# Kernel tuning notes

Hardware: AMD Instinct MI355X
Metric: run time of the kernel (lower is better)

## Reference

```python
import jax, jax.numpy as jnp
import numpy as np

B, T, NX = 2, 2048, 512
H = 2                    # n_head (structurally forced to 2 by rns() broadcasting)
L = 64                   # num landmarks (cfg.MODEL.LANDMARK)
K = 32                   # rns neighbors per token
HD = NX // H // 2        # differential head dim = 128
EPS = 1e-5


def setup_inputs() -> dict:
    key = jax.random.key(0)
    ks = jax.random.split(key, 16)
    inp = {}
    inp["x"] = jax.random.normal(ks[0], (B, T, NX), jnp.float32)
    # linear weights (torch nn.Linear stores [out,in], applies x @ W.T)
    inp["wq"] = jax.random.normal(ks[1], (NX, NX), jnp.float32) * 0.02
    inp["wk"] = jax.random.normal(ks[2], (NX, NX), jnp.float32) * 0.02
    inp["wv"] = jax.random.normal(ks[3], (NX, NX), jnp.float32) * 0.02
    inp["wo"] = jax.random.normal(ks[4], (NX, NX), jnp.float32) * 0.02
    # landmark modulation params (kaiming-normal-ish init)
    inp["m1"] = jax.random.normal(ks[5], (2 * H, L, 1), jnp.float32)
    inp["m2"] = jax.random.normal(ks[6], (2 * H, 1, L), jnp.float32)
    # differential-attention lambda params
    inp["lq1"] = jax.random.normal(ks[7], (HD,), jnp.float32) * 0.1
    inp["lk1"] = jax.random.normal(ks[8], (HD,), jnp.float32) * 0.1
    inp["lq2"] = jax.random.normal(ks[9], (HD,), jnp.float32) * 0.1
    inp["lk2"] = jax.random.normal(ks[10], (HD,), jnp.float32) * 0.1
    inp["rms_g"] = jnp.ones((2 * HD,), jnp.float32)
    inp["l"] = 3  # layer depth for lambda_init_fn
    inp["num_landmark"] = L
    inp["rns_indices"] = jax.random.randint(ks[11], (B, T, K), 0, T)
    # random.sample(range(t), L) -> distinct indices
    inp["landmark"] = jax.random.permutation(ks[12], T)[:L]
    return inp


def _forward(x, wq, wk, wv, wo, m1, m2, lq1, lk1, lq2, lk2, rms_g,
             l, rns_indices, landmark):
    b, t, nx = x.shape
    hd = nx // H // 2
    q = x @ wq.T
    k = x @ wk.T
    v = x @ wv.T
    qh = q.reshape(b, t, 2 * H, hd).transpose(0, 2, 1, 3)   # [b,2H,t,hd]
    kh = k.reshape(b, t, 2 * H, hd).transpose(0, 2, 3, 1)   # [b,2H,hd,t]
    vh = v.reshape(b, t, H, 2 * hd).transpose(0, 2, 1, 3)   # [b,H,t,2hd]

    # landmark (Nystrom) low-rank factors, L2-normalized over head dim
    sq = qh[:, :, landmark, :]                               # [b,2H,L,hd]
    sk = kh[:, :, :, landmark]                               # [b,2H,hd,L]
    sq = sq / jnp.linalg.norm(sq, axis=3, keepdims=True)
    sk = sk / jnp.linalg.norm(sk, axis=2, keepdims=True)
    sq = m1[None] * sq
    sk = m2[None] * sk

    w1 = jnp.matmul(qh, sk)                                  # [b,2H,t,L]
    w2 = jnp.matmul(sq, kh)                                  # [b,2H,L,t]
    w = jnp.matmul(w1, w2)                                   # [b,2H,t,t]

    lam_init = 0.8 - 0.6 * np.exp(-0.3 * l)
    lam = jnp.exp(jnp.sum(lq1 * lk1)) - jnp.exp(jnp.sum(lq2 * lk2)) + lam_init

    # rns symmetric sparse mask: mask[b,i,j]=1 iff j in rns_indices[b,i] AND i in rns_indices[b,j]
    bi = jnp.arange(b)[:, None, None]
    ti = jnp.arange(t)[None, :, None]
    m = jnp.zeros((b, t, t), x.dtype).at[bi, ti, rns_indices].set(1.0)
    m = m * m.transpose(0, 2, 1)
    m4 = m[:, None]                                          # broadcast over heads

    p = jax.nn.softmax(w * m4 - 1e9 * (1.0 - m4), axis=-1)   # [b,2H,t,t]
    p5 = p.reshape(b, H, 2, t, t)
    # differential mixing (note: second term indexes the HEAD dim, requires H==2)
    wmix = (p5[:, :, 0] - lam * p5[:, :, 1]) + ((1.0 - lam) * p5[:, 1] - p5[:, 0])
    a = jnp.matmul(wmix, vh)                                 # [b,H,t,2hd]

    # RMSNorm sub-layer + (1 - lambda_init) scaling
    a = a * jax.lax.rsqrt(jnp.mean(a * a, axis=-1, keepdims=True) + EPS) * rms_g
    a = a * (1.0 - lam_init)
    return a.transpose(0, 2, 1, 3).reshape(b, t, H * 2 * hd) @ wo.T


def reference(x, wq, wk, wv, wo, m1, m2, lq1, lk1, lq2, lk2, rms_g,
              l, num_landmark, rns_indices, landmark):
    return _forward(x, wq, wk, wv, wo, m1, m2, lq1, lk1, lq2, lk2, rms_g,
                    l, rns_indices, landmark)
```

## Files before the change

### kernel.cpp

```cpp
#include <hip/hip_runtime.h>
#include <hip/hip_bf16.h>

#define BB 2
#define TT 2048
#define NX 512
#define NH 4
#define HD 128
#define LL 64
#define KK 32

typedef __bf16 bf16x8 __attribute__((ext_vector_type(8)));
typedef float f32x4 __attribute__((ext_vector_type(4)));
typedef unsigned short us;
typedef const unsigned int __attribute__((address_space(1)))* gptr_t;
typedef unsigned int __attribute__((address_space(3)))* lptr_t;

__device__ __forceinline__ us f2bf(float f) {
    unsigned u = __float_as_uint(f);
    unsigned r = (u + 0x7fffu + ((u >> 16) & 1u)) >> 16;
    return (us)r;
}
__device__ __forceinline__ float bf2f(us h) {
    return __uint_as_float(((unsigned)h) << 16);
}

__global__ void k_split_all(const float* __restrict__ x,
                            const float* __restrict__ wq, const float* __restrict__ wk,
                            const float* __restrict__ wv, const float* __restrict__ wo,
                            us* __restrict__ x_hi, us* __restrict__ x_lo,
                            us* __restrict__ wqkv_hi, us* __restrict__ wqkv_lo,
                            us* __restrict__ wo_hi, us* __restrict__ wo_lo,
                            const float* __restrict__ lq1, const float* __restrict__ lk1,
                            const float* __restrict__ lq2, const float* __restrict__ lk2,
                            const int* __restrict__ lint, float* __restrict__ scal,
                            float* __restrict__ cs)
{
    const int bidx = blockIdx.x;
    if (bidx == 3072) {
        const int tid = threadIdx.x;
        const f32x4 z = {0.f, 0.f, 0.f, 0.f};
        *reinterpret_cast<f32x4*>(cs + tid * 4) = z;
        if (tid < 64) {
            float s1 = lq1[tid] * lk1[tid] + lq1[tid + 64] * lk1[tid + 64];
            float s2 = lq2[tid] * lk2[tid] + lq2[tid + 64] * lk2[tid + 64];
            for (int off = 32; off; off >>= 1) { s1 += __shfl_xor(s1, off); s2 += __shfl_xor(s2, off); }
            if (tid == 0) {
                float lam_init = 0.8f - 0.6f * expf(-0.3f * (float)lint[0]);
                scal[0] = expf(s1) - expf(s2) + lam_init;
                scal[1] = lam_init;
            }
        }
        return;
    }
    const float* src;
    us* hi;
    us* lo;
    int pos;
    if (bidx < 2048) {
        src = x; hi = x_hi; lo = x_lo;
        pos = bidx * 1024 + threadIdx.x * 4;
    } else {
        const int w = (bidx - 2048) >> 8;
        const int p = (bidx - 2048) & 255;
        pos = p * 1024 + threadIdx.x * 4;
        if (w == 0)      { src = wq; hi = wqkv_hi;          lo = wqkv_lo; }
        else if (w == 1) { src = wk; hi = wqkv_hi + 262144; lo = wqkv_lo + 262144; }
        else if (w == 2) { src = wv; hi = wqkv_hi + 524288; lo = wqkv_lo + 524288; }
        else             { src = wo; hi = wo_hi;            lo = wo_lo; }
    }
    const float4 v = *reinterpret_cast<const float4*>(src + pos);
    ushort4 h, l;
    h.x = f2bf(v.x); l.x = f2bf(v.x - bf2f(h.x));
    h.y = f2bf(v.y); l.y = f2bf(v.y - bf2f(h.y));
    h.z = f2bf(v.z); l.z = f2bf(v.z - bf2f(h.z));
    h.w = f2bf(v.w); l.w = f2bf(v.w - bf2f(h.w));
    *reinterpret_cast<ushort4*>(hi + pos) = h;
    *reinterpret_cast<ushort4*>(lo + pos) = l;
}

template<int BN, int MODE>
__global__ __launch_bounds__(256) void k_gemm_big(
    const us* __restrict__ a_hi, const us* __restrict__ a_lo,
    const us* __restrict__ b_hi, const us* __restrict__ b_lo,
    us* __restrict__ vb, float* __restrict__ cout,
    us* __restrict__ qs_hi, us* __restrict__ qs_lo,
    us* __restrict__ ks_hi, us* __restrict__ ks_lo)
{
    constexpr int NB = BN / 32;
    __shared__ us lsA[64 * 64];
    __shared__ us lsB[BN * 64];
    const int tid = threadIdx.x;
    const int m0 = blockIdx.x * 64, n0 = blockIdx.y * BN;
    const int region = n0 >> 9;
    const int ncol0 = n0 & 511;
    const int l = tid & 63, wid = tid >> 6;
    const int wr = (wid >> 1) * 32, wc = (wid & 1) * (BN / 2);
    const int lr = l & 15;
    const int lkb = (l >> 4) * 16;
    f32x4 acc[2][NB] = {};

    const int r8 = tid >> 3;
    const int swzc8 = (((tid & 7) ^ (r8 & 7)) * 8);

    const int nstep = (MODE == 0) ? (region < 2 ? 24 : 16) : 8;
    for (int kt = 0; kt < nstep; ++kt) {
        const int seg = kt >> 3;
        const int koff = (kt & 7) * 64;
        const us* ab;
        const us* bb;
        if constexpr (MODE == 0) {
            if (region < 2) {
                ab = (seg < 2 ? a_hi : a_lo) + koff + swzc8;
                bb = (seg == 1 ? b_lo : b_hi) + koff + swzc8;
            } else {
                ab = (seg == 0 ? a_hi : a_lo) + koff + swzc8;
                bb = b_hi + koff + swzc8;
            }
        } else {
            ab = a_hi + koff + swzc8;
            bb = b_hi + koff + swzc8;
        }
        #pragma unroll
        for (int j = 0; j < 2; ++j)
            __builtin_amdgcn_global_load_lds((gptr_t)(ab + (size_t)(m0 + j * 32 + r8) * 512),
                                             (lptr_t)(lsA + j * 2048 + tid * 8), 16, 0, 0);
        #pragma unroll
        for (int j = 0; j < BN / 32; ++j)
            __builtin_amdgcn_global_load_lds((gptr_t)(bb + (size_t)(n0 + j * 32 + r8) * 512),
                                             (lptr_t)(lsB + j * 2048 + tid * 8), 16, 0, 0);
        __syncthreads();
        bf16x8 af[2][2], bfr[NB][2];
        #pragma unroll
        for (int m = 0; m < 2; ++m) {
            const int row = wr + m * 16 + lr;
            #pragma unroll
            for (int kk = 0; kk < 2; ++kk) {
                const int cb = (kk * 64 + lkb) ^ ((row & 7) << 4);
                af[m][kk] = *reinterpret_cast<const bf16x8*>(
                    (const char*)lsA + row * 128 + cb);
            }
        }
        #pragma unroll
        for (int n = 0; n < NB; ++n) {
            const int row = wc + n * 16 + lr;
            #pragma unroll
            for (int kk = 0; kk < 2; ++kk) {
                const int cb = (kk * 64 + lkb) ^ ((row & 7) << 4);
                bfr[n][kk] = *reinterpret_cast<const bf16x8*>(
                    (const char*)lsB + row * 128 + cb);
            }
        }
        #pragma unroll
        for (int kk = 0; kk < 2; ++kk)
            #pragma unroll
            for (int m = 0; m < 2; ++m)
                #pragma unroll
                for (int n = 0; n < NB; ++n)
                    acc[m][n] = __builtin_amdgcn_mfma_f32_16x16x32_bf16(
                        af[m][kk], bfr[n][kk], acc[m][n], 0, 0, 0);
        __syncthreads();
    }

    if constexpr (MODE == 0) {
        if (region < 2) {
            us* sh = (region == 0) ? qs_hi : ks_hi;
            us* slo = (region == 0) ? qs_lo : ks_lo;
            #pragma unroll
            for (int m = 0; m < 2; ++m) {
                const int row = m0 + wr + m * 16 + (l >> 4) * 4;
                #pragma unroll
                for (int n = 0; n < NB; ++n) {
                    const int col = ncol0 + wc + n * 16 + lr;
                    #pragma unroll
                    for (int r = 0; r < 4; ++r) {
                        const float val = acc[m][n][r];
                        const us h = f2bf(val);
                        sh[(size_t)(row + r) * 512 + col] = h;
                        slo[(size_t)(row + r) * 512 + col] = f2bf(val - bf2f(h));
                    }
                }
            }
        } else {
            #pragma unroll
            for (int m = 0; m < 2; ++m) {
                const int row = m0 + wr + m * 16 + (l >> 4) * 4;
                #pragma unroll
                for (int n = 0; n < NB; ++n) {
                    const int col = ncol0 + wc + n * 16 + lr;
                    #pragma unroll
                    for (int r = 0; r < 4; ++r)
                        vb[(size_t)(row + r) * 512 + col] = f2bf(acc[m][n][r]);
                }
            }
        }
    } else {
        #pragma unroll
        for (int m = 0; m < 2; ++m) {
            const int row = m0 + wr + m * 16 + (l >> 4) * 4;
            #pragma unroll
            for (int n = 0; n < NB; ++n) {
                const int col = n0 + wc + n * 16 + lr;
                #pragma unroll
                for (int r = 0; r < 4; ++r)
                    cout[(size_t)(row + r) * 512 + col] = acc[m][n][r];
            }
        }
    }
}

__global__ __launch_bounds__(256) void k_w12_colsum(
    const us* __restrict__ q_hi, const us* __restrict__ q_lo,
    const us* __restrict__ k_hi, const us* __restrict__ k_lo,
    const us* __restrict__ kn_hi, const us* __restrict__ kn_lo,
    const us* __restrict__ qn_hi, const us* __restrict__ qn_lo,
    float* __restrict__ w1, float* __restrict__ w2t,
    const us* __restrict__ vb, float* __restrict__ cs)
{
    const int blk = blockIdx.x;
    const int tid = threadIdx.x;
    if (blk >= 384) {
        const int c4 = tid * 4;
        const int b = c4 >> 9, c = c4 & 511;
        const int t0 = (blk - 384) * 64;
        const us* p = vb + ((size_t)(b * TT + t0)) * NX + c;
        f32x4 s = {0.f, 0.f, 0.f, 0.f};
        for (int t = 0; t < 64; ++t) {
            const ushort4 u = *reinterpret_cast<const ushort4*>(p + (size_t)t * NX);
            s[0] += bf2f(u.x); s[1] += bf2f(u.y); s[2] += bf2f(u.z); s[3] += bf2f(u.w);
        }
        atomicAdd(&cs[c4 + 0], s[0]);
        atomicAdd(&cs[c4 + 1], s[1]);
        atomicAdd(&cs[c4 + 2], s[2]);
        atomicAdd(&cs[c4 + 3], s[3]);
        return;
    }
    __shared__ us lsA[64 * 32];
    __shared__ us lsB[64 * 32];
    const int m0 = (blk & 31) * 64;
    const int y = (blk >> 5) % 6;
    const int z = blk / 192;
    const int hh = y % 3, b = y / 3;
    const int h = hh + 1;
    const us* ah = (z ? k_hi : q_hi) + ((size_t)b * 2048) * 512 + h * 128;
    const us* al = (z ? k_lo : q_lo) + ((size_t)b * 2048) * 512 + h * 128;
    const us* bhp = (z ? qn_hi : kn_hi) + (size_t)(b * 4 + h) * 64 * 128;
    const us* blp = (z ? qn_lo : kn_lo) + (size_t)(b * 4 + h) * 64 * 128;
    float* C = (z ? w2t : w1) + (size_t)(b * 3 + hh) * 2048 * 64;

    const int l = tid & 63, wid = tid >> 6;
    const int wr = (wid >> 1) * 32, wc = (wid & 1) * 32;
    const int lr = l & 15, lk8 = (l >> 4) * 8;
    f32x4 acc[2][2] = {};
    const int srow = tid >> 2, scol = (tid & 3) * 8;

    for (int kt = 0; kt < 12; ++kt) {
        const int seg = kt >> 2;
        const int koff = (kt & 3) * 32;
        const us* ab = (seg < 2 ? ah : al) + koff + scol;
        const us* bb = (seg == 1 ? blp : bhp) + koff + scol;
        __builtin_amdgcn_global_load_lds((gptr_t)(ab + (size_t)(m0 + srow) * 512),
                                         (lptr_t)(lsA + tid * 8), 16, 0, 0);
        __builtin_amdgcn_global_load_lds((gptr_t)(bb + (size_t)srow * 128),
                                         (lptr_t)(lsB + tid * 8), 16, 0, 0);
        __syncthreads();
        bf16x8 af[2], bfr[2];
        #pragma unroll
        for (int m = 0; m < 2; ++m)
            af[m] = *reinterpret_cast<const bf16x8*>(&lsA[(wr + m * 16 + lr) * 32 + lk8]);
        #pragma unroll
        for (int n = 0; n < 2; ++n)
            bfr[n] = *reinterpret_cast<const bf16x8*>(&lsB[(wc + n * 16 + lr) * 32 + lk8]);
        #pragma unroll
        for (int m = 0; m < 2; ++m)
            #pragma unroll
            for (int n = 0; n < 2; ++n)
                acc[m][n] = __builtin_amdgcn_mfma_f32_16x16x32_bf16(af[m], bfr[n], acc[m][n], 0, 0, 0);
        __syncthreads();
    }

    #pragma unroll
    for (int m = 0; m < 2; ++m) {
        const int row = m0 + wr + m * 16 + (l >> 4) * 4;
        #pragma unroll
        for (int n = 0; n < 2; ++n) {
            const int col = wc + n * 16 + lr;
            #pragma unroll
            for (int r = 0; r < 4; ++r)
                C[(size_t)(row + r) * 64 + col] = acc[m][n][r];
        }
    }
}

__global__ __launch_bounds__(256) void k_norm_lm(
    const us* __restrict__ q_hi, const us* __restrict__ q_lo,
    const us* __restrict__ k_hi, const us* __restrict__ k_lo,
    const float* __restrict__ m1, const float* __restrict__ m2,
    const int* __restrict__ landmark,
    us* __restrict__ qn_hi, us* __restrict__ qn_lo,
    us* __restrict__ kn_hi, us* __restrict__ kn_lo)
{
    const int idx = blockIdx.x * 4 + (threadIdx.x >> 6);
    const int l = idx & 63;
    const int h = (idx >> 6) & 3;
    const int b = idx >> 8;
    const int lm = landmark[l];
    const int d = threadIdx.x & 63;

    const size_t qoff = ((size_t)(b * TT + lm)) * NX + h * HD;
    const float qa = bf2f(q_hi[qoff + d]) + bf2f(q_lo[qoff + d]);
    const float qb = bf2f(q_hi[qoff + d + 64]) + bf2f(q_lo[qoff + d + 64]);
    const float ka = bf2f(k_hi[qoff + d]) + bf2f(k_lo[qoff + d]);
    const float kb = bf2f(k_hi[qoff + d + 64]) + bf2f(k_lo[qoff + d + 64]);
    float sq = qa * qa + qb * qb;
    float sk = ka * ka + kb * kb;
    for (int off = 32; off; off >>= 1) { sq += __shfl_xor(sq, off); sk += __shfl_xor(sk, off); }
    const float invq = rsqrtf(sq) * m1[h * LL + l];
    const float invk = rsqrtf(sk) * m2[h * LL + l];
    const size_t base = (((size_t)(b * NH + h)) * LL + l) * HD;
    const float vq0 = qa * invq, vq1 = qb * invq;
    const float vk0 = ka * invk, vk1 = kb * invk;
    us h0;
    h0 = f2bf(vq0); qn_hi[base + d] = h0;      qn_lo[base + d] = f2bf(vq0 - bf2f(h0));
    h0 = f2bf(vq1); qn_hi[base + d + 64] = h0; qn_lo[base + d + 64] = f2bf(vq1 - bf2f(h0));
    h0 = f2bf(vk0); kn_hi[base + d] = h0;      kn_lo[base + d] = f2bf(vk0 - bf2f(h0));
    h0 = f2bf(vk1); kn_hi[base + d + 64] = h0; kn_lo[base + d + 64] = f2bf(vk1 - bf2f(h0));
}

__global__ __launch_bounds__(256) void k_sparse_attn(
    const float* __restrict__ w1, const float* __restrict__ w2t,
    const us* __restrict__ vb, const float* __restrict__ cs,
    const int* __restrict__ rns, const float* __restrict__ rms_g,
    const float* __restrict__ scal,
    us* __restrict__ ao)
{
    const int wid = threadIdx.x >> 6;
    const int lane = threadIdx.x & 63;
    const int bi = blockIdx.x * 4 + wid;
    const int b = bi >> 11, i = bi & 2047;

    __shared__ int   sl[4][32];
    __shared__ float plog[4][96];
    __shared__ float wmm[4][2][32];
    __shared__ float w1s[4][3][64];

    const int myidx = lane & 31;
    const int cand = rns[(size_t)bi * KK + myidx];
    int dup = 0;
    #pragma unroll
    for (int kk = 0; kk < 31; ++kk) {
        const int other = __shfl(cand, kk);
        dup |= (kk < myidx) & (other == cand);
    }
    const int* jrow = rns + ((size_t)(b * TT + cand)) * KK + (lane >> 5) * 16;
    int found = 0;
    #pragma unroll
    for (int kk = 0; kk < 16; ++kk) found |= (jrow[kk] == i);
    found |= __shfl_xor(found, 32);
    const int keep = (!dup) && found;
    const unsigned long long mask = __ballot(keep) & 0xffffffffull;
    const int sc = __popcll(mask);
    const int pos = __popcll(mask & ((1ull << myidx) - 1ull));
    if (lane < 32 && keep) sl[wid][pos] = cand;

    const float lam = scal[0], lam_init = scal[1];

    if (sc > 0) {
        #pragma unroll
        for (int r = 0; r < 3; ++r)
            w1s[wid][r][lane] = w1[(((size_t)(b * 3 + r)) * TT + i) * LL + lane];
        const int ntask = 3 * sc;
        for (int t0 = 0; t0 < ntask; t0 += 8) {
            const int t = t0 + (lane >> 3);
            float part = 0.f;
            if (t < ntask) {
                const int hh = t % 3, ss = t / 3;
                const int j = sl[wid][ss];
                const float* w2row = w2t + (((size_t)(b * 3 + hh)) * TT + j) * LL + (lane & 7) * 8;
                const float* w1p = &w1s[wid][hh][(lane & 7) * 8];
                #pragma unroll
                for (int e = 0; e < 8; ++e) part += w1p[e] * w2row[e];
            }
            part += __shfl_xor(part, 1);
            part += __shfl_xor(part, 2);
            part += __shfl_xor(part, 4);
            if (t < ntask && (lane & 7) == 0) plog[wid][t] = part;
        }
        if (lane < 3) {
            float mx = -1e30f;
            for (int ss = 0; ss < sc; ++ss) mx = fmaxf(mx, plog[wid][ss * 3 + lane]);
            float s = 0.f;
            for (int ss = 0; ss < sc; ++ss) {
                const float e = expf(plog[wid][ss * 3 + lane] - mx);
                plog[wid][ss * 3 + lane] = e;
                s += e;
            }
            const float inv = 1.0f / s;
            for (int ss = 0; ss < sc; ++ss) plog[wid][ss * 3 + lane] *= inv;
        }
        if (lane < sc) {
            const float p1 = plog[wid][lane * 3 + 0];
            const float p2 = plog[wid][lane * 3 + 1];
            const float p3 = plog[wid][lane * 3 + 2];
            wmm[wid][0][lane] = (1.0f - lam) * p2 - lam * p1;
            wmm[wid][1][lane] = p2 - p1 + (1.0f - 2.0f * lam) * p3;
        }
    }

    f32x4 acc0 = {0.f, 0.f, 0.f, 0.f}, acc1 = {0.f, 0.f, 0.f, 0.f};
    if (sc == 0) {
        const float cc = (1.0f - 2.0f * lam) * (1.0f / (float)TT);
        const f32x4 c0 = *reinterpret_cast<const f32x4*>(cs + b * NX + lane * 4);
        const f32x4 c1 = *reinterpret_cast<const f32x4*>(cs + b * NX + 256 + lane * 4);
        acc0 = cc * c0;
        acc1 = cc * c1;
    } else {
        for (int ss = 0; ss < sc; ++ss) {
            const float wa = wmm[wid][0][ss], wb = wmm[wid][1][ss];
            const us* vrow = vb + ((size_t)(b * TT + sl[wid][ss])) * NX;
            const ushort4 ua = *reinterpret_cast<const ushort4*>(vrow + lane * 4);
            const ushort4 ub = *reinterpret_cast<const ushort4*>(vrow + 256 + lane * 4);
            acc0[0] += wa * bf2f(ua.x); acc0[1] += wa * bf2f(ua.y);
            acc0[2] += wa * bf2f(ua.z); acc0[3] += wa * bf2f(ua.w);
            acc1[0] += wb * bf2f(ub.x); acc1[1] += wb * bf2f(ub.y);
            acc1[2] += wb * bf2f(ub.z); acc1[3] += wb * bf2f(ub.w);
        }
    }

    float s0 = acc0[0]*acc0[0] + acc0[1]*acc0[1] + acc0[2]*acc0[2] + acc0[3]*acc0[3];
    float s1 = acc1[0]*acc1[0] + acc1[1]*acc1[1] + acc1[2]*acc1[2] + acc1[3]*acc1[3];
    #pragma unroll
    for (int off = 32; off; off >>= 1) { s0 += __shfl_xor(s0, off); s1 += __shfl_xor(s1, off); }
    const float sc0 = rsqrtf(s0 * (1.0f / 256.0f) + 1e-5f);
    const float sc1 = rsqrtf(s1 * (1.0f / 256.0f) + 1e-5f);
    const float og = 1.0f - lam_init;
    const f32x4 g = *reinterpret_cast<const f32x4*>(rms_g + lane * 4);
    ushort4 h0, h1;
    #pragma unroll
    for (int e = 0; e < 4; ++e) {
        (&h0.x)[e] = f2bf(acc0[e] * sc0 * g[e] * og);
        (&h1.x)[e] = f2bf(acc1[e] * sc1 * g[e] * og);
    }
    *reinterpret_cast<ushort4*>(ao + (size_t)bi * NX + lane * 4) = h0;
    *reinterpret_cast<ushort4*>(ao + (size_t)bi * NX + 256 + lane * 4) = h1;
}

extern "C" void kernel_launch(void* const* d_in, const int* in_sizes, int n_in,
                              void* d_out, int out_size, void* d_ws, size_t ws_size,
                              hipStream_t stream)
{
    const float* x    = (const float*)d_in[0];
    const float* wq   = (const float*)d_in[1];
    const float* wk   = (const float*)d_in[2];
    const float* wv   = (const float*)d_in[3];
    const float* wo   = (const float*)d_in[4];
    const float* m1   = (const float*)d_in[5];
    const float* m2   = (const float*)d_in[6];
    const float* lq1  = (const float*)d_in[7];
    const float* lk1  = (const float*)d_in[8];
    const float* lq2  = (const float*)d_in[9];
    const float* lk2  = (const float*)d_in[10];
    const float* rmsg = (const float*)d_in[11];
    const int*   lint = (const int*)d_in[12];
    const int*   rns  = (const int*)d_in[14];
    const int*   lmk  = (const int*)d_in[15];
    float* out = (float*)d_out;
    float* ws  = (float*)d_ws;

    const size_t M2 = 2097152;
    const size_t W3 = 786432;
    float* w1   = ws;
    float* w2t  = ws + W3;
    float* cs   = ws + 2 * W3;
    float* scal = cs + 1024;
    us* S = (us*)(scal + 128);
    us* vb   = S;
    us* x_hi = S + M2;
    us* x_lo = S + 2 * M2;
    us* ao   = x_hi;
    us* q_hi = S + 3 * M2;
    us* q_lo = S + 4 * M2;
    us* k_hi = S + 5 * M2;
    us* k_lo = S + 6 * M2;
    us* wqkv_hi = S + 7 * M2;
    us* wqkv_lo = wqkv_hi + 786432;
    us* wo_hi = wqkv_lo + 786432;
    us* wo_lo = wo_hi + 262144;
    us* qn_hi = wo_lo + 262144;
    us* qn_lo = qn_hi + 65536;
    us* kn_hi = qn_lo + 65536;
    us* kn_lo = kn_hi + 65536;

    k_split_all<<<3073, 256, 0, stream>>>(x, wq, wk, wv, wo,
                                          x_hi, x_lo, wqkv_hi, wqkv_lo, wo_hi, wo_lo,
                                          lq1, lk1, lq2, lk2, lint, scal, cs);

    k_gemm_big<128, 0><<<dim3(64, 12), 256, 0, stream>>>(
        x_hi, x_lo, wqkv_hi, wqkv_lo, vb, nullptr, q_hi, q_lo, k_hi, k_lo);

    k_norm_lm<<<128, 256, 0, stream>>>(q_hi, q_lo, k_hi, k_lo, m1, m2, lmk,
                                       qn_hi, qn_lo, kn_hi, kn_lo);
    k_w12_colsum<<<416, 256, 0, stream>>>(q_hi, q_lo, k_hi, k_lo,
                                          kn_hi, kn_lo, qn_hi, qn_lo, w1, w2t, vb, cs);
    k_sparse_attn<<<1024, 256, 0, stream>>>(w1, w2t, vb, cs, rns, rmsg, scal, ao);

    k_gemm_big<64, 1><<<dim3(64, 8), 256, 0, stream>>>(
        ao, nullptr, wo_hi, nullptr, nullptr, out, nullptr, nullptr, nullptr, nullptr);
}
```

Measured before the change: 141.1 us.

## Fold landmark factors into weights to skip full Q/K projections

The full Q and K projections are no longer computed. Only the landmark rows of Q/K are projected, normalized, and multiplied into the Wq/Wk weights to form effective weights, so the Nystrom factors w1/w2 come straight from x times those weights. Separate V and output GEMM kernels replace the templated one, and the hi/lo splitting of Wv and Wo is dropped. This removes the large Q/K GEMM and its split-precision outputs. In exchange it adds several small serial kernels (the landmark GEMM with only 16 blocks, norm, weff) and changes the rounding path.

```diff
diff --git a/kernel.cpp b/kernel.cpp
--- a/kernel.cpp
+++ b/kernel.cpp
@@ -28,8 +28,9 @@
                             const float* __restrict__ wq, const float* __restrict__ wk,
                             const float* __restrict__ wv, const float* __restrict__ wo,
                             us* __restrict__ x_hi, us* __restrict__ x_lo,
-                            us* __restrict__ wqkv_hi, us* __restrict__ wqkv_lo,
-                            us* __restrict__ wo_hi, us* __restrict__ wo_lo,
+                            us* __restrict__ wq_hi, us* __restrict__ wq_lo,
+                            us* __restrict__ wk_hi, us* __restrict__ wk_lo,
+                            us* __restrict__ wv_hi, us* __restrict__ wo_hi,
                             const float* __restrict__ lq1, const float* __restrict__ lk1,
                             const float* __restrict__ lq2, const float* __restrict__ lk2,
                             const int* __restrict__ lint, float* __restrict__ scal,
@@ -54,7 +55,7 @@
     }
     const float* src;
     us* hi;
-    us* lo;
+    us* lo = nullptr;
     int pos;
     if (bidx < 2048) {
         src = x; hi = x_hi; lo = x_lo;
@@ -63,91 +64,72 @@
         const int w = (bidx - 2048) >> 8;
         const int p = (bidx - 2048) & 255;
         pos = p * 1024 + threadIdx.x * 4;
-        if (w == 0)      { src = wq; hi = wqkv_hi;          lo = wqkv_lo; }
-        else if (w == 1) { src = wk; hi = wqkv_hi + 262144; lo = wqkv_lo + 262144; }
-        else if (w == 2) { src = wv; hi = wqkv_hi + 524288; lo = wqkv_lo + 524288; }
-        else             { src = wo; hi = wo_hi;            lo = wo_lo; }
+        if (w == 0)      { src = wq; hi = wq_hi; lo = wq_lo; }
+        else if (w == 1) { src = wk; hi = wk_hi; lo = wk_lo; }
+        else if (w == 2) { src = wv; hi = wv_hi; }
+        else             { src = wo; hi = wo_hi; }
     }
     const float4 v = *reinterpret_cast<const float4*>(src + pos);
-    ushort4 h, l;
-    h.x = f2bf(v.x); l.x = f2bf(v.x - bf2f(h.x));
-    h.y = f2bf(v.y); l.y = f2bf(v.y - bf2f(h.y));
-    h.z = f2bf(v.z); l.z = f2bf(v.z - bf2f(h.z));
-    h.w = f2bf(v.w); l.w = f2bf(v.w - bf2f(h.w));
+    ushort4 h;
+    h.x = f2bf(v.x); h.y = f2bf(v.y); h.z = f2bf(v.z); h.w = f2bf(v.w);
     *reinterpret_cast<ushort4*>(hi + pos) = h;
-    *reinterpret_cast<ushort4*>(lo + pos) = l;
-}
-
-template<int BN, int MODE>
-__global__ __launch_bounds__(256) void k_gemm_big(
-    const us* __restrict__ a_hi, const us* __restrict__ a_lo,
-    const us* __restrict__ b_hi, const us* __restrict__ b_lo,
-    us* __restrict__ vb, float* __restrict__ cout,
-    us* __restrict__ qs_hi, us* __restrict__ qs_lo,
-    us* __restrict__ ks_hi, us* __restrict__ ks_lo)
-{
-    constexpr int NB = BN / 32;
+    if (lo) {
+        ushort4 l;
+        l.x = f2bf(v.x - bf2f(h.x));
+        l.y = f2bf(v.y - bf2f(h.y));
+        l.z = f2bf(v.z - bf2f(h.z));
+        l.w = f2bf(v.w - bf2f(h.w));
+        *reinterpret_cast<ushort4*>(lo + pos) = l;
+    }
+}
+
+__global__ __launch_bounds__(256) void k_gemm_v(
+    const us* __restrict__ x_hi, const us* __restrict__ x_lo,
+    const us* __restrict__ wv_hi, us* __restrict__ vb)
+{
     __shared__ us lsA[64 * 64];
-    __shared__ us lsB[BN * 64];
+    __shared__ us lsB[128 * 64];
     const int tid = threadIdx.x;
-    const int m0 = blockIdx.x * 64, n0 = blockIdx.y * BN;
-    const int region = n0 >> 9;
-    const int ncol0 = n0 & 511;
+    const int m0 = blockIdx.x * 64, n0 = blockIdx.y * 128;
     const int l = tid & 63, wid = tid >> 6;
-    const int wr = (wid >> 1) * 32, wc = (wid & 1) * (BN / 2);
+    const int wr = (wid >> 1) * 32, wc = (wid & 1) * 64;
     const int lr = l & 15;
     const int lkb = (l >> 4) * 16;
-    f32x4 acc[2][NB] = {};
-
+    f32x4 acc[2][4] = {};
     const int r8 = tid >> 3;
     const int swzc8 = (((tid & 7) ^ (r8 & 7)) * 8);
 
-    const int nstep = (MODE == 0) ? (region < 2 ? 24 : 16) : 8;
-    for (int kt = 0; kt < nstep; ++kt) {
+    for (int kt = 0; kt < 16; ++kt) {
         const int seg = kt >> 3;
         const int koff = (kt & 7) * 64;
-        const us* ab;
-        const us* bb;
-        if constexpr (MODE == 0) {
-            if (region < 2) {
-                ab = (seg < 2 ? a_hi : a_lo) + koff + swzc8;
-                bb = (seg == 1 ? b_lo : b_hi) + koff + swzc8;
-            } else {
-                ab = (seg == 0 ? a_hi : a_lo) + koff + swzc8;
-                bb = b_hi + koff + swzc8;
-            }
-        } else {
-            ab = a_hi + koff + swzc8;
-            bb = b_hi + koff + swzc8;
-        }
+        const us* ab = (seg == 0 ? x_hi : x_lo) + koff + swzc8;
+        const us* bb = wv_hi + koff + swzc8;
         #pragma unroll
         for (int j = 0; j < 2; ++j)
             __builtin_amdgcn_global_load_lds((gptr_t)(ab + (size_t)(m0 + j * 32 + r8) * 512),
                                              (lptr_t)(lsA + j * 2048 + tid * 8), 16, 0, 0);
         #pragma unroll
-        for (int j = 0; j < BN / 32; ++j)
+        for (int j = 0; j < 4; ++j)
             __builtin_amdgcn_global_load_lds((gptr_t)(bb + (size_t)(n0 + j * 32 + r8) * 512),
                                              (lptr_t)(lsB + j * 2048 + tid * 8), 16, 0, 0);
         __syncthreads();
-        bf16x8 af[2][2], bfr[NB][2];
+        bf16x8 af[2][2], bfr[4][2];
         #pragma unroll
         for (int m = 0; m < 2; ++m) {
             const int row = wr + m * 16 + lr;
             #pragma unroll
             for (int kk = 0; kk < 2; ++kk) {
                 const int cb = (kk * 64 + lkb) ^ ((row & 7) << 4);
-                af[m][kk] = *reinterpret_cast<const bf16x8*>(
-                    (const char*)lsA + row * 128 + cb);
-            }
-        }
-        #pragma unroll
-        for (int n = 0; n < NB; ++n) {
+                af[m][kk] = *reinterpret_cast<const bf16x8*>((const char*)lsA + row * 128 + cb);
+            }
+        }
+        #pragma unroll
+        for (int n = 0; n < 4; ++n) {
             const int row = wc + n * 16 + lr;
             #pragma unroll
             for (int kk = 0; kk < 2; ++kk) {
                 const int cb = (kk * 64 + lkb) ^ ((row & 7) << 4);
-                bfr[n][kk] = *reinterpret_cast<const bf16x8*>(
-                    (const char*)lsB + row * 128 + cb);
+                bfr[n][kk] = *reinterpret_cast<const bf16x8*>((const char*)lsB + row * 128 + cb);
             }
         }
         #pragma unroll
@@ -155,77 +137,208 @@
             #pragma unroll
             for (int m = 0; m < 2; ++m)
                 #pragma unroll
-                for (int n = 0; n < NB; ++n)
+                for (int n = 0; n < 4; ++n)
                     acc[m][n] = __builtin_amdgcn_mfma_f32_16x16x32_bf16(
                         af[m][kk], bfr[n][kk], acc[m][n], 0, 0, 0);
         __syncthreads();
     }
 
-    if constexpr (MODE == 0) {
-        if (region < 2) {
-            us* sh = (region == 0) ? qs_hi : ks_hi;
-            us* slo = (region == 0) ? qs_lo : ks_lo;
-            #pragma unroll
-            for (int m = 0; m < 2; ++m) {
-                const int row = m0 + wr + m * 16 + (l >> 4) * 4;
+    #pragma unroll
+    for (int m = 0; m < 2; ++m) {
+        const int row = m0 + wr + m * 16 + (l >> 4) * 4;
+        #pragma unroll
+        for (int n = 0; n < 4; ++n) {
+            const int col = n0 + wc + n * 16 + lr;
+            #pragma unroll
+            for (int r = 0; r < 4; ++r)
+                vb[(size_t)(row + r) * 512 + col] = f2bf(acc[m][n][r]);
+        }
+    }
+}
+
+__global__ __launch_bounds__(256) void k_sqk(
+    const us* __restrict__ x_hi, const us* __restrict__ x_lo,
+    const us* __restrict__ wq_hi, const us* __restrict__ wq_lo,
+    const us* __restrict__ wk_hi, const us* __restrict__ wk_lo,
+    const int* __restrict__ lmk, float* __restrict__ sqk)
+{
+    __shared__ us lsA[64 * 64];
+    __shared__ us lsB[128 * 64];
+    const int tid = threadIdx.x;
+    const int bq = blockIdx.x;
+    const int n0 = blockIdx.y * 128;
+    const us* bhi = (n0 < 512) ? wq_hi : wk_hi;
+    const us* blo = (n0 < 512) ? wq_lo : wk_lo;
+    const int ncol = n0 & 511;
+    const int l = tid & 63, wid = tid >> 6;
+    const int wr = (wid >> 1) * 32, wc = (wid & 1) * 64;
+    const int lr = l & 15;
+    const int lkb = (l >> 4) * 16;
+    f32x4 acc[2][4] = {};
+    const int r8 = tid >> 3;
+    const int swzc8 = (((tid & 7) ^ (r8 & 7)) * 8);
+
+    for (int kt = 0; kt < 24; ++kt) {
+        const int seg = kt >> 3;
+        const int koff = (kt & 7) * 64;
+        const us* ab = (seg < 2 ? x_hi : x_lo) + koff + swzc8;
+        const us* bb = (seg == 1 ? blo : bhi) + koff + swzc8;
+        #pragma unroll
+        for (int j = 0; j < 2; ++j) {
+            const int arow = bq * TT + lmk[j * 32 + r8];
+            __builtin_amdgcn_global_load_lds((gptr_t)(ab + (size_t)arow * 512),
+                                             (lptr_t)(lsA + j * 2048 + tid * 8), 16, 0, 0);
+        }
+        #pragma unroll
+        for (int j = 0; j < 4; ++j)
+            __builtin_amdgcn_global_load_lds((gptr_t)(bb + (size_t)(ncol + j * 32 + r8) * 512),
+                                             (lptr_t)(lsB + j * 2048 + tid * 8), 16, 0, 0);
+        __syncthreads();
+        bf16x8 af[2][2], bfr[4][2];
+        #pragma unroll
+        for (int m = 0; m < 2; ++m) {
+            const int row = wr + m * 16 + lr;
+            #pragma unroll
+            for (int kk = 0; kk < 2; ++kk) {
+                const int cb = (kk * 64 + lkb) ^ ((row & 7) << 4);
+                af[m][kk] = *reinterpret_cast<const bf16x8*>((const char*)lsA + row * 128 + cb);
+            }
+        }
+        #pragma unroll
+        for (int n = 0; n < 4; ++n) {
+            const int row = wc + n * 16 + lr;
+            #pragma unroll
+            for (int kk = 0; kk < 2; ++kk) {
+                const int cb = (kk * 64 + lkb) ^ ((row & 7) << 4);
+                bfr[n][kk] = *reinterpret_cast<const bf16x8*>((const char*)lsB + row * 128 + cb);
+            }
+        }
+        #pragma unroll
+        for (int kk = 0; kk < 2; ++kk)
+            #pragma unroll
+            for (int m = 0; m < 2; ++m)
                 #pragma unroll
-                for (int n = 0; n < NB; ++n) {
-                    const int col = ncol0 + wc + n * 16 + lr;
-                    #pragma unroll
-                    for (int r = 0; r < 4; ++r) {
-                        const float val = acc[m][n][r];
-                        const us h = f2bf(val);
-                        sh[(size_t)(row + r) * 512 + col] = h;
-                        slo[(size_t)(row + r) * 512 + col] = f2bf(val - bf2f(h));
-                    }
-                }
-            }
-        } else {
-            #pragma unroll
-            for (int m = 0; m < 2; ++m) {
-                const int row = m0 + wr + m * 16 + (l >> 4) * 4;
-                #pragma unroll
-                for (int n = 0; n < NB; ++n) {
-                    const int col = ncol0 + wc + n * 16 + lr;
-                    #pragma unroll
-                    for (int r = 0; r < 4; ++r)
-                        vb[(size_t)(row + r) * 512 + col] = f2bf(acc[m][n][r]);
-                }
-            }
-        }
-    } else {
-        #pragma unroll
-        for (int m = 0; m < 2; ++m) {
-            const int row = m0 + wr + m * 16 + (l >> 4) * 4;
-            #pragma unroll
-            for (int n = 0; n < NB; ++n) {
-                const int col = n0 + wc + n * 16 + lr;
-                #pragma unroll
-                for (int r = 0; r < 4; ++r)
-                    cout[(size_t)(row + r) * 512 + col] = acc[m][n][r];
-            }
+                for (int n = 0; n < 4; ++n)
+                    acc[m][n] = __builtin_amdgcn_mfma_f32_16x16x32_bf16(
+                        af[m][kk], bfr[n][kk], acc[m][n], 0, 0, 0);
+        __syncthreads();
+    }
+
+    #pragma unroll
+    for (int m = 0; m < 2; ++m) {
+        const int rowl = wr + m * 16 + (l >> 4) * 4;
+        #pragma unroll
+        for (int n = 0; n < 4; ++n) {
+            const int col = n0 + wc + n * 16 + lr;
+            #pragma unroll
+            for (int r = 0; r < 4; ++r)
+                sqk[(size_t)(bq * 64 + rowl + r) * 1024 + col] = acc[m][n][r];
+        }
+    }
+}
+
+__global__ __launch_bounds__(256) void k_norm(
+    const float* __restrict__ sqk, const float* __restrict__ m1,
+    const float* __restrict__ m2, float* __restrict__ qn, float* __restrict__ kn)
+{
+    const int u = blockIdx.x * 4 + (threadIdx.x >> 6);
+    const int l = u & 63;
+    const int hh = (u >> 6) % 3;
+    const int b = u / 192;
+    const int h = hh + 1;
+    const int d = threadIdx.x & 63;
+
+    const float* qrow = sqk + (size_t)(b * 64 + l) * 1024 + h * HD;
+    const float* krow = qrow + 512;
+    const float qa = qrow[d], qb = qrow[d + 64];
+    const float ka = krow[d], kb = krow[d + 64];
+    float sq = qa * qa + qb * qb;
+    float sk = ka * ka + kb * kb;
+    for (int off = 32; off; off >>= 1) { sq += __shfl_xor(sq, off); sk += __shfl_xor(sk, off); }
+    const float invq = rsqrtf(sq) * m1[h * LL + l];
+    const float invk = rsqrtf(sk) * m2[h * LL + l];
+    const size_t base = ((size_t)(b * 3 + hh) * 64 + l) * HD;
+    qn[base + d] = qa * invq;  qn[base + d + 64] = qb * invq;
+    kn[base + d] = ka * invk;  kn[base + d + 64] = kb * invk;
+}
+
+__global__ __launch_bounds__(256) void k_weff(
+    const float* __restrict__ qn, const float* __restrict__ kn,
+    const float* __restrict__ wq, const float* __restrict__ wk,
+    us* __restrict__ weff_hi, us* __restrict__ weff_lo)
+{
+    __shared__ float As[64][128];
+    __shared__ float Ws[128][64];
+    const int blk = blockIdx.x;
+    const int c8 = blk & 7;
+    const int t = blk >> 3;
+    const int hh = t % 3;
+    const int z = (t / 3) & 1;
+    const int b = t / 6;
+    const int h = hh + 1;
+    const int tid = threadIdx.x;
+
+    const float* A = (z ? qn : kn) + (size_t)(b * 3 + hh) * 64 * 128;
+    const float* W = (z ? wk : wq) + (size_t)h * 128 * 512 + c8 * 64;
+
+    #pragma unroll
+    for (int it = 0; it < 8; ++it) {
+        const int f = (it * 256 + tid) * 4;
+        *reinterpret_cast<f32x4*>(&As[f >> 7][f & 127]) =
+            *reinterpret_cast<const f32x4*>(A + f);
+    }
+    #pragma unroll
+    for (int it = 0; it < 8; ++it) {
+        const int f = (it * 256 + tid) * 4;
+        const int d = f >> 6, c = f & 63;
+        *reinterpret_cast<f32x4*>(&Ws[d][c]) =
+            *reinterpret_cast<const f32x4*>(W + (size_t)d * 512 + c);
+    }
+    __syncthreads();
+
+    const int tx = tid & 15, ty = tid >> 4;
+    float acc[4][4] = {};
+    for (int d = 0; d < 128; ++d) {
+        const float a0 = As[ty * 4 + 0][d], a1 = As[ty * 4 + 1][d];
+        const float a2 = As[ty * 4 + 2][d], a3 = As[ty * 4 + 3][d];
+        const float w0 = Ws[d][tx * 4 + 0], w1v = Ws[d][tx * 4 + 1];
+        const float w2v = Ws[d][tx * 4 + 2], w3 = Ws[d][tx * 4 + 3];
+        acc[0][0] += a0 * w0; acc[0][1] += a0 * w1v; acc[0][2] += a0 * w2v; acc[0][3] += a0 * w3;
+        acc[1][0] += a1 * w0; acc[1][1] += a1 * w1v; acc[1][2] += a1 * w2v; acc[1][3] += a1 * w3;
+        acc[2][0] += a2 * w0; acc[2][1] += a2 * w1v; acc[2][2] += a2 * w2v; acc[2][3] += a2 * w3;
+        acc[3][0] += a3 * w0; acc[3][1] += a3 * w1v; acc[3][2] += a3 * w2v; acc[3][3] += a3 * w3;
+    }
+
+    const size_t rowbase = (size_t)(b * 384 + z * 192 + hh * 64);
+    #pragma unroll
+    for (int i = 0; i < 4; ++i) {
+        const size_t row = rowbase + ty * 4 + i;
+        #pragma unroll
+        for (int j = 0; j < 4; ++j) {
+            const size_t off = row * 512 + c8 * 64 + tx * 4 + j;
+            const float val = acc[i][j];
+            const us hv = f2bf(val);
+            weff_hi[off] = hv;
+            weff_lo[off] = f2bf(val - bf2f(hv));
         }
     }
 }
 
 __global__ __launch_bounds__(256) void k_w12_colsum(
-    const us* __restrict__ q_hi, const us* __restrict__ q_lo,
-    const us* __restrict__ k_hi, const us* __restrict__ k_lo,
-    const us* __restrict__ kn_hi, const us* __restrict__ kn_lo,
-    const us* __restrict__ qn_hi, const us* __restrict__ qn_lo,
-    float* __restrict__ w1, float* __restrict__ w2t,
-    const us* __restrict__ vb, float* __restrict__ cs)
+    const us* __restrict__ x_hi, const us* __restrict__ x_lo,
+    const us* __restrict__ weff_hi, const us* __restrict__ weff_lo,
+    float* __restrict__ w12, const us* __restrict__ vb, float* __restrict__ cs)
 {
     const int blk = blockIdx.x;
     const int tid = threadIdx.x;
-    if (blk >= 384) {
+    if (blk >= 192) {
         const int c4 = tid * 4;
         const int b = c4 >> 9, c = c4 & 511;
-        const int t0 = (blk - 384) * 64;
+        const int t0 = (blk - 192) * 64;
         const us* p = vb + ((size_t)(b * TT + t0)) * NX + c;
         f32x4 s = {0.f, 0.f, 0.f, 0.f};
-        for (int t = 0; t < 64; ++t) {
-            const ushort4 u = *reinterpret_cast<const ushort4*>(p + (size_t)t * NX);
+        for (int tt = 0; tt < 64; ++tt) {
+            const ushort4 u = *reinterpret_cast<const ushort4*>(p + (size_t)tt * NX);
             s[0] += bf2f(u.x); s[1] += bf2f(u.y); s[2] += bf2f(u.z); s[3] += bf2f(u.w);
         }
         atomicAdd(&cs[c4 + 0], s[0]);
@@ -234,103 +347,89 @@
         atomicAdd(&cs[c4 + 3], s[3]);
         return;
     }
-    __shared__ us lsA[64 * 32];
-    __shared__ us lsB[64 * 32];
-    const int m0 = (blk & 31) * 64;
-    const int y = (blk >> 5) % 6;
-    const int z = blk / 192;
-    const int hh = y % 3, b = y / 3;
-    const int h = hh + 1;
-    const us* ah = (z ? k_hi : q_hi) + ((size_t)b * 2048) * 512 + h * 128;
-    const us* al = (z ? k_lo : q_lo) + ((size_t)b * 2048) * 512 + h * 128;
-    const us* bhp = (z ? qn_hi : kn_hi) + (size_t)(b * 4 + h) * 64 * 128;
-    const us* blp = (z ? qn_lo : kn_lo) + (size_t)(b * 4 + h) * 64 * 128;
-    float* C = (z ? w2t : w1) + (size_t)(b * 3 + hh) * 2048 * 64;
+    __shared__ us lsA[64 * 64];
+    __shared__ us lsB[128 * 64];
+    const int bx = blk & 31;
+    const int ny = (blk >> 5) % 3;
+    const int b = blk / 96;
+    const int m0 = b * TT + bx * 64;
+    const int n0b = ny * 128;
+    const us* bhi = weff_hi + (size_t)b * 384 * 512;
+    const us* blo = weff_lo + (size_t)b * 384 * 512;
 
     const int l = tid & 63, wid = tid >> 6;
-    const int wr = (wid >> 1) * 32, wc = (wid & 1) * 32;
-    const int lr = l & 15, lk8 = (l >> 4) * 8;
-    f32x4 acc[2][2] = {};
-    const int srow = tid >> 2, scol = (tid & 3) * 8;
-
-    for (int kt = 0; kt < 12; ++kt) {
-        const int seg = kt >> 2;
-        const int koff = (kt & 3) * 32;
-        const us* ab = (seg < 2 ? ah : al) + koff + scol;
-        const us* bb = (seg == 1 ? blp : bhp) + koff + scol;
-        __builtin_amdgcn_global_load_lds((gptr_t)(ab + (size_t)(m0 + srow) * 512),
-                                         (lptr_t)(lsA + tid * 8), 16, 0, 0);
-        __builtin_amdgcn_global_load_lds((gptr_t)(bb + (size_t)srow * 128),
-                                         (lptr_t)(lsB + tid * 8), 16, 0, 0);
-        __syncthreads();
-        bf16x8 af[2], bfr[2];
-        #pragma unroll
-        for (int m = 0; m < 2; ++m)
-            af[m] = *reinterpret_cast<const bf16x8*>(&lsA[(wr + m * 16 + lr) * 32 + lk8]);
-        #pragma unroll
-        for (int n = 0; n < 2; ++n)
-            bfr[n] = *reinterpret_cast<const bf16x8*>(&lsB[(wc + n * 16 + lr) * 32 + lk8]);
-        #pragma unroll
-        for (int m = 0; m < 2; ++m)
-            #pragma unroll
-            for (int n = 0; n < 2; ++n)
-                acc[m][n] = __builtin_amdgcn_mfma_f32_16x16x32_bf16(af[m], bfr[n], acc[m][n], 0, 0, 0);
+    const int wr = (wid >> 1) * 32, wc = (wid & 1) * 64;
+    const int lr = l & 15;
+    const int lkb = (l >> 4) * 16;
+    f32x4 acc[2][4] = {};
+    const int r8 = tid >> 3;
+    const int swzc8 = (((tid & 7) ^ (r8 & 7)) * 8);
+
+    for (int kt = 0; kt < 24; ++kt) {
+        const int seg = kt >> 3;
+        const int koff = (kt & 7) * 64;
+        const us* ab = (seg < 2 ? x_hi : x_lo) + koff + swzc8;
+        const us* bb = (seg == 1 ? blo : bhi) + koff + swzc8;
+        #pragma unroll
+        for (int j = 0; j < 2; ++j)
+            __builtin_amdgcn_global_load_lds((gptr_t)(ab + (size_t)(m0 + j * 32 + r8) * 512),
+                                             (lptr_t)(lsA + j * 2048 + tid * 8), 16, 0, 0);
+        #pragma unroll
+        for (int j = 0; j < 4; ++j)
+            __builtin_amdgcn_global_load_lds((gptr_t)(bb + (size_t)(n0b + j * 32 + r8) * 512),
+                                             (lptr_t)(lsB + j * 2048 + tid * 8), 16, 0, 0);
+        __syncthreads();
+        bf16x8 af[2][2], bfr[4][2];
+        #pragma unroll
+        for (int m = 0; m < 2; ++m) {
+            const int row = wr + m * 16 + lr;
+            #pragma unroll
+            for (int kk = 0; kk < 2; ++kk) {
+                const int cb = (kk * 64 + lkb) ^ ((row & 7) << 4);
+                af[m][kk] = *reinterpret_cast<const bf16x8*>((const char*)lsA + row * 128 + cb);
+            }
+        }
+        #pragma unroll
+        for (int n = 0; n < 4; ++n) {
+            const int row = wc + n * 16 + lr;
+            #pragma unroll
+            for (int kk = 0; kk < 2; ++kk) {
+                const int cb = (kk * 64 + lkb) ^ ((row & 7) << 4);
+                bfr[n][kk] = *reinterpret_cast<const bf16x8*>((const char*)lsB + row * 128 + cb);
+            }
+        }
+        #pragma unroll
+        for (int kk = 0; kk < 2; ++kk)
+            #pragma unroll
+            for (int m = 0; m < 2; ++m)
+                #pragma unroll
+                for (int n = 0; n < 4; ++n)
+                    acc[m][n] = __builtin_amdgcn_mfma_f32_16x16x32_bf16(
+                        af[m][kk], bfr[n][kk], acc[m][n], 0, 0, 0);
         __syncthreads();
     }
 
     #pragma unroll
     for (int m = 0; m < 2; ++m) {
-        const int row = m0 + wr + m * 16 + (l >> 4) * 4;
-        #pragma unroll
-        for (int n = 0; n < 2; ++n) {
-            const int col = wc + n * 16 + lr;
+        const int i = bx * 64 + wr + m * 16 + (l >> 4) * 4;
+        #pragma unroll
+        for (int n = 0; n < 4; ++n) {
+            const int col = n0b + wc + n * 16 + lr;
+            const int z = col / 192;
+            const int r2 = col - z * 192;
+            const int hh = r2 >> 6, ll = r2 & 63;
+            float* C = w12 + (((size_t)((b * 2 + z) * 3 + hh) * TT)) * 64;
             #pragma unroll
             for (int r = 0; r < 4; ++r)
-                C[(size_t)(row + r) * 64 + col] = acc[m][n][r];
-        }
-    }
-}
-
-__global__ __launch_bounds__(256) void k_norm_lm(
-    const us* __restrict__ q_hi, const us* __restrict__ q_lo,
-    const us* __restrict__ k_hi, const us* __restrict__ k_lo,
-    const float* __restrict__ m1, const float* __restrict__ m2,
-    const int* __restrict__ landmark,
-    us* __restrict__ qn_hi, us* __restrict__ qn_lo,
-    us* __restrict__ kn_hi, us* __restrict__ kn_lo)
-{
-    const int idx = blockIdx.x * 4 + (threadIdx.x >> 6);
-    const int l = idx & 63;
-    const int h = (idx >> 6) & 3;
-    const int b = idx >> 8;
-    const int lm = landmark[l];
-    const int d = threadIdx.x & 63;
-
-    const size_t qoff = ((size_t)(b * TT + lm)) * NX + h * HD;
-    const float qa = bf2f(q_hi[qoff + d]) + bf2f(q_lo[qoff + d]);
-    const float qb = bf2f(q_hi[qoff + d + 64]) + bf2f(q_lo[qoff + d + 64]);
-    const float ka = bf2f(k_hi[qoff + d]) + bf2f(k_lo[qoff + d]);
-    const float kb = bf2f(k_hi[qoff + d + 64]) + bf2f(k_lo[qoff + d + 64]);
-    float sq = qa * qa + qb * qb;
-    float sk = ka * ka + kb * kb;
-    for (int off = 32; off; off >>= 1) { sq += __shfl_xor(sq, off); sk += __shfl_xor(sk, off); }
-    const float invq = rsqrtf(sq) * m1[h * LL + l];
-    const float invk = rsqrtf(sk) * m2[h * LL + l];
-    const size_t base = (((size_t)(b * NH + h)) * LL + l) * HD;
-    const float vq0 = qa * invq, vq1 = qb * invq;
-    const float vk0 = ka * invk, vk1 = kb * invk;
-    us h0;
-    h0 = f2bf(vq0); qn_hi[base + d] = h0;      qn_lo[base + d] = f2bf(vq0 - bf2f(h0));
-    h0 = f2bf(vq1); qn_hi[base + d + 64] = h0; qn_lo[base + d + 64] = f2bf(vq1 - bf2f(h0));
-    h0 = f2bf(vk0); kn_hi[base + d] = h0;      kn_lo[base + d] = f2bf(vk0 - bf2f(h0));
-    h0 = f2bf(vk1); kn_hi[base + d + 64] = h0; kn_lo[base + d + 64] = f2bf(vk1 - bf2f(h0));
+                C[(size_t)(i + r) * 64 + ll] = acc[m][n][r];
+        }
+    }
 }
 
 __global__ __launch_bounds__(256) void k_sparse_attn(
-    const float* __restrict__ w1, const float* __restrict__ w2t,
-    const us* __restrict__ vb, const float* __restrict__ cs,
-    const int* __restrict__ rns, const float* __restrict__ rms_g,
-    const float* __restrict__ scal,
+    const float* __restrict__ w12, const us* __restrict__ vb,
+    const float* __restrict__ cs, const int* __restrict__ rns,
+    const float* __restrict__ rms_g, const float* __restrict__ scal,
     us* __restrict__ ao)
 {
     const int wid = threadIdx.x >> 6;
@@ -363,11 +462,13 @@
     if (lane < 32 && keep) sl[wid][pos] = cand;
 
     const float lam = scal[0], lam_init = scal[1];
+    const float* w1b = w12 + (size_t)(b * 2) * 3 * TT * 64;
+    const float* w2b = w12 + (size_t)(b * 2 + 1) * 3 * TT * 64;
 
     if (sc > 0) {
         #pragma unroll
         for (int r = 0; r < 3; ++r)
-            w1s[wid][r][lane] = w1[(((size_t)(b * 3 + r)) * TT + i) * LL + lane];
+            w1s[wid][r][lane] = w1b[((size_t)r * TT + i) * 64 + lane];
         const int ntask = 3 * sc;
         for (int t0 = 0; t0 < ntask; t0 += 8) {
             const int t = t0 + (lane >> 3);
@@ -375,7 +476,7 @@
             if (t < ntask) {
                 const int hh = t % 3, ss = t / 3;
                 const int j = sl[wid][ss];
-                const float* w2row = w2t + (((size_t)(b * 3 + hh)) * TT + j) * LL + (lane & 7) * 8;
+                const float* w2row = w2b + ((size_t)hh * TT + j) * 64 + (lane & 7) * 8;
                 const float* w1p = &w1s[wid][hh][(lane & 7) * 8];
                 #pragma unroll
                 for (int e = 0; e < 8; ++e) part += w1p[e] * w2row[e];
@@ -444,6 +545,76 @@
     *reinterpret_cast<ushort4*>(ao + (size_t)bi * NX + 256 + lane * 4) = h1;
 }
 
+__global__ __launch_bounds__(256) void k_gemm_out(
+    const us* __restrict__ ao, const us* __restrict__ wo_hi, float* __restrict__ out)
+{
+    __shared__ us lsA[64 * 64];
+    __shared__ us lsB[64 * 64];
+    const int tid = threadIdx.x;
+    const int m0 = blockIdx.x * 64, n0 = blockIdx.y * 64;
+    const int l = tid & 63, wid = tid >> 6;
+    const int wr = (wid >> 1) * 32, wc = (wid & 1) * 32;
+    const int lr = l & 15;
+    const int lkb = (l >> 4) * 16;
+    f32x4 acc[2][2] = {};
+    const int r8 = tid >> 3;
+    const int swzc8 = (((tid & 7) ^ (r8 & 7)) * 8);
+
+    for (int kt = 0; kt < 8; ++kt) {
+        const int koff = kt * 64;
+        const us* ab = ao + koff + swzc8;
+        const us* bb = wo_hi + koff + swzc8;
+        #pragma unroll
+        for (int j = 0; j < 2; ++j) {
+            __builtin_amdgcn_global_load_lds((gptr_t)(ab + (size_t)(m0 + j * 32 + r8) * 512),
+                                             (lptr_t)(lsA + j * 2048 + tid * 8), 16, 0, 0);
+            __builtin_amdgcn_global_load_lds((gptr_t)(bb + (size_t)(n0 + j * 32 + r8) * 512),
+                                             (lptr_t)(lsB + j * 2048 + tid * 8), 16, 0, 0);
+        }
+        __syncthreads();
+        bf16x8 af[2][2], bfr[2][2];
+        #pragma unroll
+        for (int m = 0; m < 2; ++m) {
+            const int row = wr + m * 16 + lr;
+            #pragma unroll
+            for (int kk = 0; kk < 2; ++kk) {
+                const int cb = (kk * 64 + lkb) ^ ((row & 7) << 4);
+                af[m][kk] = *reinterpret_cast<const bf16x8*>((const char*)lsA + row * 128 + cb);
+            }
+        }
+        #pragma unroll
+        for (int n = 0; n < 2; ++n) {
+            const int row = wc + n * 16 + lr;
+            #pragma unroll
+            for (int kk = 0; kk < 2; ++kk) {
+                const int cb = (kk * 64 + lkb) ^ ((row & 7) << 4);
+                bfr[n][kk] = *reinterpret_cast<const bf16x8*>((const char*)lsB + row * 128 + cb);
+            }
+        }
+        #pragma unroll
+        for (int kk = 0; kk < 2; ++kk)
+            #pragma unroll
+            for (int m = 0; m < 2; ++m)
+                #pragma unroll
+                for (int n = 0; n < 2; ++n)
+                    acc[m][n] = __builtin_amdgcn_mfma_f32_16x16x32_bf16(
+                        af[m][kk], bfr[n][kk], acc[m][n], 0, 0, 0);
+        __syncthreads();
+    }
+
+    #pragma unroll
+    for (int m = 0; m < 2; ++m) {
+        const int row = m0 + wr + m * 16 + (l >> 4) * 4;
+        #pragma unroll
+        for (int n = 0; n < 2; ++n) {
+            const int col = n0 + wc + n * 16 + lr;
+            #pragma unroll
+            for (int r = 0; r < 4; ++r)
+                out[(size_t)(row + r) * 512 + col] = acc[m][n][r];
+        }
+    }
+}
+
 extern "C" void kernel_launch(void* const* d_in, const int* in_sizes, int n_in,
                               void* d_out, int out_size, void* d_ws, size_t ws_size,
                               hipStream_t stream)
@@ -466,43 +637,42 @@
     float* out = (float*)d_out;
     float* ws  = (float*)d_ws;
 
-    const size_t M2 = 2097152;
-    const size_t W3 = 786432;
-    float* w1   = ws;
-    float* w2t  = ws + W3;
-    float* cs   = ws + 2 * W3;
+    float* w12  = ws;
+    float* sqk  = ws + 1572864;
+    float* qn   = sqk + 131072;
+    float* kn   = qn + 49152;
+    float* cs   = kn + 49152;
     float* scal = cs + 1024;
     us* S = (us*)(scal + 128);
-    us* vb   = S;
-    us* x_hi = S + M2;
-    us* x_lo = S + 2 * M2;
-    us* ao   = x_hi;
-    us* q_hi = S + 3 * M2;
-    us* q_lo = S + 4 * M2;
-    us* k_hi = S + 5 * M2;
-    us* k_lo = S + 6 * M2;
-    us* wqkv_hi = S + 7 * M2;
-    us* wqkv_lo = wqkv_hi + 786432;
-    us* wo_hi = wqkv_lo + 786432;
-    us* wo_lo = wo_hi + 262144;
-    us* qn_hi = wo_lo + 262144;
-    us* qn_lo = qn_hi + 65536;
-    us* kn_hi = qn_lo + 65536;
-    us* kn_lo = kn_hi + 65536;
+    const size_t M2 = 2097152;
+    us* vb      = S;
+    us* x_hi    = S + M2;
+    us* x_lo    = S + 2 * M2;
+    us* ao      = x_hi;
+    us* wq_hi   = S + 3 * M2;
+    us* wq_lo   = wq_hi + 262144;
+    us* wk_hi   = wq_lo + 262144;
+    us* wk_lo   = wk_hi + 262144;
+    us* wv_hi   = wk_lo + 262144;
+    us* wo_hi   = wv_hi + 262144;
+    us* weff_hi = wo_hi + 262144;
+    us* weff_lo = weff_hi + 393216;
 
     k_split_all<<<3073, 256, 0, stream>>>(x, wq, wk, wv, wo,
-                                          x_hi, x_lo, wqkv_hi, wqkv_lo, wo_hi, wo_lo,
+                                          x_hi, x_lo, wq_hi, wq_lo, wk_hi, wk_lo,
+                                          wv_hi, wo_hi,
                                           lq1, lk1, lq2, lk2, lint, scal, cs);
 
-    k_gemm_big<128, 0><<<dim3(64, 12), 256, 0, stream>>>(
-        x_hi, x_lo, wqkv_hi, wqkv_lo, vb, nullptr, q_hi, q_lo, k_hi, k_lo);
-
-    k_norm_lm<<<128, 256, 0, stream>>>(q_hi, q_lo, k_hi, k_lo, m1, m2, lmk,
-                                       qn_hi, qn_lo, kn_hi, kn_lo);
-    k_w12_colsum<<<416, 256, 0, stream>>>(q_hi, q_lo, k_hi, k_lo,
-                                          kn_hi, kn_lo, qn_hi, qn_lo, w1, w2t, vb, cs);
-    k_sparse_attn<<<1024, 256, 0, stream>>>(w1, w2t, vb, cs, rns, rmsg, scal, ao);
-
-    k_gemm_big<64, 1><<<dim3(64, 8), 256, 0, stream>>>(
-        ao, nullptr, wo_hi, nullptr, nullptr, out, nullptr, nullptr, nullptr, nullptr);
-}
+    k_gemm_v<<<dim3(64, 4), 256, 0, stream>>>(x_hi, x_lo, wv_hi, vb);
+
+    k_sqk<<<dim3(2, 8), 256, 0, stream>>>(x_hi, x_lo, wq_hi, wq_lo, wk_hi, wk_lo,
+                                          lmk, sqk);
+    k_norm<<<96, 256, 0, stream>>>(sqk, m1, m2, qn, kn);
+    k_weff<<<96, 256, 0, stream>>>(qn, kn, wq, wk, weff_hi, weff_lo);
+
+    k_w12_colsum<<<224, 256, 0, stream>>>(x_hi, x_lo, weff_hi, weff_lo, w12, vb, cs);
+
+    k_sparse_attn<<<1024, 256, 0, stream>>>(w12, vb, cs, rns, rmsg, scal, ao);
+
+    k_gemm_out<<<dim3(64, 8), 256, 0, stream>>>(ao, wo_hi, out);
+}
```

New measurement: 171.2 us. 1.21x slower.
